# Optimization experiments

Measured on AMD Instinct MI355X. Metric: run time of the kernel, lower is better.

The kernel has to match this reference:

```python
import jax, jax.numpy as jnp
import numpy as np

K = 1024          # num_embeddings
D = 768           # embedding_dim
COMMIT = 0.25     # commitment_cost
PW = 0.1          # perplexity_weight


def setup_inputs() -> dict:
    key = jax.random.key(0)
    k1, k2 = jax.random.split(key)
    inputs = jax.random.normal(k1, (32, 2048, D), dtype=jnp.float32)
    weight = jax.random.normal(k2, (K, D), dtype=jnp.float32)  # codebook
    return {"inputs": inputs, "weight": weight}


def reference(inputs, weight):
    """Eval-mode forward of VectorQuantizerEMA (deterministic nearest-code lookup)."""
    in_shape = inputs.shape
    flat = inputs.reshape(-1, D)                       # [N, D]
    valid = jnp.linalg.norm(flat, axis=1) > 1e-6       # padding mask [N]
    maskf = valid.astype(flat.dtype)
    n_valid = maskf.sum()

    dist = (jnp.sum(flat * flat, axis=1, keepdims=True)
            + jnp.sum(weight * weight, axis=1)
            - 2.0 * flat @ weight.T)

    idx = jnp.argmin(dist, axis=1)                     # [N]
    min_d = jnp.min(dist, axis=1)                      # [N]
    idx = jnp.where(valid, idx, 0)
    min_d = jnp.where(valid, min_d, 0.0)

    q_flat = weight[idx] * maskf[:, None]              # zeros at padded rows
    quantized = q_flat.reshape(in_shape)
    quantized_st = inputs + jax.lax.stop_gradient(quantized - inputs)

    # commitment loss: MSE over valid rows only
    sq_err = jnp.sum((flat - jax.lax.stop_gradient(q_flat)) ** 2, axis=1)
    loss_commit = jnp.sum(maskf * sq_err) / (n_valid * D)

    # perplexity over valid assignments (one-hot mean == normalized counts)
    counts = jnp.zeros((K,), flat.dtype).at[idx].add(maskf)
    avg_probs = counts / n_valid
    perplexity = jnp.exp(-jnp.sum(avg_probs * jnp.log(avg_probs + 1e-10)))
    perplexity_loss = -jnp.log(perplexity + 1e-10)

    total_loss = COMMIT * loss_commit + PW * perplexity_loss

    indices = idx.reshape(in_shape[:-1])
    min_distances = min_d.reshape(in_shape[:-1])
    return quantized_st, total_loss, indices, min_distances, perplexity
```

## Files before the change

kernel.cpp:

```cpp
#include <hip/hip_runtime.h>
#include <hip/hip_bf16.h>
#include <math.h>

#define NROWS 65536
#define DDIM  768
#define KCODES 1024
#define NCB   8
#define BM    128
#define BK    128
#define KC    32
#define NCH   (DDIM / KC)
#define BK2   32
#define NCH2  (DDIM / BK2)
#define PANEL_USH (24 * 4096)
#define GAP_TAU  0.3f
#define FILT_TAU 0.6f
#define RGRID 2048
#define QGRID 2048

#define OUT_LOSS ((size_t)NROWS * DDIM)
#define OUT_IDX  (OUT_LOSS + 1)
#define OUT_MIND (OUT_IDX + NROWS)
#define OUT_PERP (OUT_MIND + NROWS)

#define WS_SUM    0
#define WS_NSUS   8
#define WS_NVAL   12
#define WS_COUNTS 256
#define WS_WSQ    (WS_COUNTS + 4*KCODES)
#define WS_ROWS   (WS_WSQ + 4*KCODES)
#define WS_ROWI   (WS_ROWS + 4*NROWS)
#define WS_SUSP   (WS_ROWI + 4*NROWS)
#define WS_PM1    (WS_SUSP + 4*NROWS)
#define WS_PM2    (WS_PM1 + (size_t)4*NROWS*NCB)
#define WS_PIDX   (WS_PM2 + (size_t)4*NROWS*NCB)
#define WS_END    (WS_PIDX + (size_t)4*NROWS*NCB)
#define WS_AF16   ((WS_END + 255) & ~(size_t)255)
#define WS_WF16   (WS_AF16 + (size_t)NROWS * DDIM * 2)
#define WS_END2   (WS_WF16 + (size_t)KCODES * DDIM * 2)

typedef __attribute__((ext_vector_type(8))) _Float16 half8;
typedef __attribute__((ext_vector_type(4))) float f32x4;

#define GLOAD16(gsrc, ldst) \
    __builtin_amdgcn_global_load_lds( \
        (const __attribute__((address_space(1))) unsigned int*)(gsrc), \
        (__attribute__((address_space(3))) unsigned int*)(ldst), 16, 0, 0)

template <typename T>
__device__ inline T waveRedAdd(T v) {
#pragma unroll
    for (int o = 32; o; o >>= 1) v += __shfl_xor(v, o);
    return v;
}

__device__ inline ushort f2h(float f) {
    union { _Float16 h; ushort u; } c;
    c.h = (_Float16)f;
    return c.u;
}

__global__ void k_init(float* counts, int* n_suspect, unsigned* n_valid, double* sum_sqerr) {
    const int t = threadIdx.x;
    if (t == 0) { *n_suspect = 0; *n_valid = 0u; *sum_sqerr = 0.0; }
    for (int k = t; k < KCODES; k += 256) counts[k] = 0.f;
}

#define ASLOTS (NROWS * (DDIM / 8))
#define TSLOTS ((NROWS + KCODES) * (DDIM / 8))
__global__ __launch_bounds__(256) void k_convert(
    const float* __restrict__ A, const float* __restrict__ W,
    ushort* __restrict__ Af16, ushort* __restrict__ Wf16)
{
    for (int gidx = blockIdx.x * 256 + threadIdx.x; gidx < TSLOTS; gidx += gridDim.x * 256) {
        const float* src; ushort* dst; int sid;
        if (gidx < ASLOTS) { src = A; dst = Af16; sid = gidx; }
        else { src = W; dst = Wf16; sid = gidx - ASLOTS; }
        const int row = sid / 96;
        const int sl = sid - row * 96;
        const int ch = sl >> 2, s = sl & 3;
        const float* p = src + (size_t)row * DDIM + ch * 32 + s * 8;
        const float4 a = *(const float4*)p;
        const float4 b = *(const float4*)(p + 4);
        uint4 v;
        v.x = ((unsigned)f2h(a.y) << 16) | f2h(a.x);
        v.y = ((unsigned)f2h(a.w) << 16) | f2h(a.z);
        v.z = ((unsigned)f2h(b.y) << 16) | f2h(b.x);
        v.w = ((unsigned)f2h(b.w) << 16) | f2h(b.z);
        const size_t dsti = (size_t)(row >> 7) * PANEL_USH + ch * 4096
                          + (row & 127) * 32 + ((s ^ ((row >> 1) & 3)) << 3);
        *(uint4*)(dst + dsti) = v;
    }
}

__global__ __launch_bounds__(256) void k_wsq(const float* __restrict__ W, float* __restrict__ wsq) {
    const int k = blockIdx.x;
    const int t = threadIdx.x;
    const float* w = W + (size_t)k * DDIM;
    const float a = w[t], b = w[t + 256], c = w[t + 512];
    float s = a * a + b * b + c * c;
    s = waveRedAdd(s);
    __shared__ float p[4];
    if ((t & 63) == 0) p[t >> 6] = s;
    __syncthreads();
    if (t == 0) wsq[k] = (p[0] + p[1]) + (p[2] + p[3]);
}

__global__ __launch_bounds__(256, 4) void k_partials_g(
    const ushort* __restrict__ Af16, const ushort* __restrict__ Wf16,
    const float* __restrict__ wsq,
    float* __restrict__ pm1, float* __restrict__ pm2, int* __restrict__ pidx)
{
    __shared__ __align__(16) ushort lds[2 * 2 * BM * BK2];

    const int bid = blockIdx.x;
    const int rb = ((bid & 7) << 6) | (bid >> 6);
    const int cb = (bid >> 3) & 7;

    const int tid = threadIdx.x;
    const int wid = tid >> 6, lane = tid & 63;
    const int wr = wid >> 1, wc = wid & 1;
    const int l15 = lane & 15, g = lane >> 4;

    const ushort* Ap = Af16 + (size_t)rb * PANEL_USH;
    const ushort* Wp = Wf16 + (size_t)cb * PANEL_USH;

    int aoff[4], boff[4];
#pragma unroll
    for (int rt = 0; rt < 4; ++rt) {
        const int r = wr * 64 + rt * 16 + l15;
        aoff[rt] = r * 32 + ((g ^ ((r >> 1) & 3)) << 3);
        const int c = wc * 64 + rt * 16 + l15;
        boff[rt] = c * 32 + ((g ^ ((c >> 1) & 3)) << 3);
    }

    f32x4 acc[4][4];
#pragma unroll
    for (int rt = 0; rt < 4; ++rt)
#pragma unroll
        for (int ct = 0; ct < 4; ++ct) acc[rt][ct] = (f32x4)0.f;

    const int lseg = lane << 3;
    auto STAGE = [&](int ch, int b) {
        ushort* As = lds + b * 8192;
        ushort* Ws = As + 4096;
        const ushort* Asrc = Ap + ch * 4096;
        const ushort* Wsrc = Wp + ch * 4096;
        GLOAD16(Asrc + (wid << 9) + lseg,       (char*)As + (wid << 10));
        GLOAD16(Asrc + ((wid + 4) << 9) + lseg, (char*)As + ((wid + 4) << 10));
        GLOAD16(Wsrc + (wid << 9) + lseg,       (char*)Ws + (wid << 10));
        GLOAD16(Wsrc + ((wid + 4) << 9) + lseg, (char*)Ws + ((wid + 4) << 10));
    };

    STAGE(0, 0);
    __syncthreads();

#pragma unroll 2
    for (int ch = 0; ch < NCH2; ++ch) {
        const int cur = ch & 1;
        if (ch + 1 < NCH2) STAGE(ch + 1, cur ^ 1);
        const ushort* As = lds + cur * 8192;
        const ushort* Ws = As + 4096;
        half8 bf[4];
#pragma unroll
        for (int ct = 0; ct < 4; ++ct) bf[ct] = *(const half8*)(Ws + boff[ct]);
#pragma unroll
        for (int rt = 0; rt < 4; ++rt) {
            const half8 af = *(const half8*)(As + aoff[rt]);
#pragma unroll
            for (int ct = 0; ct < 4; ++ct)
                acc[rt][ct] = __builtin_amdgcn_mfma_f32_16x16x32_f16(af, bf[ct], acc[rt][ct], 0, 0, 0);
        }
        __syncthreads();
    }

    float wq[4];
#pragma unroll
    for (int ct = 0; ct < 4; ++ct) wq[ct] = wsq[cb * BK + wc * 64 + ct * 16 + l15];
    const int cbase = cb * BK + wc * 64 + l15;

    float* tm1 = (float*)lds;
    float* tm2 = tm1 + 256;
    int*   ti1 = (int*)(tm2 + 256);

#pragma unroll
    for (int rt = 0; rt < 4; ++rt) {
        float m1q[4], m2q[4]; int i1q[4];
#pragma unroll
        for (int q = 0; q < 4; ++q) { m1q[q] = INFINITY; m2q[q] = INFINITY; i1q[q] = 0x7fffffff; }
#pragma unroll
        for (int ct = 0; ct < 4; ++ct) {
            const int col = cbase + ct * 16;
#pragma unroll
            for (int q = 0; q < 4; ++q) {
                const float s = fmaf(-2.f, acc[rt][ct][q], wq[ct]);
                if (s < m1q[q]) { m2q[q] = m1q[q]; m1q[q] = s; i1q[q] = col; }
                else if (s < m2q[q]) m2q[q] = s;
            }
        }
#pragma unroll
        for (int msk = 1; msk <= 8; msk <<= 1) {
#pragma unroll
            for (int q = 0; q < 4; ++q) {
                const float om1 = __shfl_xor(m1q[q], msk);
                const float om2 = __shfl_xor(m2q[q], msk);
                const int   oi1 = __shfl_xor(i1q[q], msk);
                if (om1 < m1q[q] || (om1 == m1q[q] && oi1 < i1q[q])) {
                    m2q[q] = fminf(m1q[q], om2); m1q[q] = om1; i1q[q] = oi1;
                } else m2q[q] = fminf(m2q[q], om1);
            }
        }
        if (l15 == 0) {
#pragma unroll
            for (int q = 0; q < 4; ++q) {
                const int rl = wr * 64 + rt * 16 + g * 4 + q;
                tm1[rl * 2 + wc] = m1q[q];
                tm2[rl * 2 + wc] = m2q[q];
                ti1[rl * 2 + wc] = i1q[q];
            }
        }
    }
    __syncthreads();
    if (tid < BM) {
        float m1 = tm1[tid * 2], m2 = tm2[tid * 2]; int i1 = ti1[tid * 2];
        const float bm1 = tm1[tid * 2 + 1], bm2 = tm2[tid * 2 + 1]; const int bi = ti1[tid * 2 + 1];
        if (bm1 < m1 || (bm1 == m1 && bi < i1)) { m2 = fminf(m1, bm2); m1 = bm1; i1 = bi; }
        else m2 = fminf(m2, bm1);
        const size_t row = (size_t)rb * BM + tid;
        pm1[row * NCB + cb] = m1;
        pm2[row * NCB + cb] = m2;
        pidx[row * NCB + cb] = i1;
    }
}

__global__ __launch_bounds__(256, 2) void k_partials(
    const float* __restrict__ A, const float* __restrict__ W,
    const float* __restrict__ wsq,
    float* __restrict__ pm1, float* __restrict__ pm2, int* __restrict__ pidx)
{
    __shared__ __align__(16) ushort lds[2 * BM * KC];
    ushort* As = lds;
    ushort* Ws = lds + BM * KC;

    const int bid = blockIdx.x;
    const int rb = ((bid & 7) << 6) | (bid >> 6);
    const int cb = (bid >> 3) & 7;

    const int tid = threadIdx.x;
    const int wid = tid >> 6, lane = tid & 63;
    const int wr = wid >> 1, wc = wid & 1;
    const int l15 = lane & 15, g = lane >> 4;

    const float* Ab = A + (size_t)rb * BM * DDIM;
    const float* Wb = W + (size_t)cb * BK * DDIM;

    const int srow = tid >> 3;
    const int sk4  = (tid & 7) << 2;
    const int sg   = (tid & 7) >> 1;
    const int sh   = (tid & 1) << 2;

    int aOff[4], bOff[4];
#pragma unroll
    for (int rt = 0; rt < 4; ++rt) {
        const int r = wr * 64 + rt * 16 + l15;
        aOff[rt] = r * KC + ((g ^ ((r >> 1) & 3)) << 3);
        const int c = wc * 64 + rt * 16 + l15;
        bOff[rt] = c * KC + ((g ^ ((c >> 1) & 3)) << 3);
    }

    f32x4 acc[4][4];
#pragma unroll
    for (int rt = 0; rt < 4; ++rt)
#pragma unroll
        for (int ct = 0; ct < 4; ++ct) acc[rt][ct] = (f32x4)0.f;

    float4 av[4], wv[4];
#pragma unroll
    for (int i = 0; i < 4; ++i) {
        av[i] = *(const float4*)(Ab + (size_t)(srow + 32 * i) * DDIM + sk4);
        wv[i] = *(const float4*)(Wb + (size_t)(srow + 32 * i) * DDIM + sk4);
    }

#pragma unroll 1
    for (int ch = 0; ch < NCH; ++ch) {
        __syncthreads();
#pragma unroll
        for (int i = 0; i < 4; ++i) {
            const int r = srow + 32 * i;
            const int wsl = r * KC + ((sg ^ ((r >> 1) & 3)) << 3) + sh;
            ushort4 ua; ua.x = f2h(av[i].x); ua.y = f2h(av[i].y); ua.z = f2h(av[i].z); ua.w = f2h(av[i].w);
            *(ushort4*)(As + wsl) = ua;
            ushort4 uw; uw.x = f2h(wv[i].x); uw.y = f2h(wv[i].y); uw.z = f2h(wv[i].z); uw.w = f2h(wv[i].w);
            *(ushort4*)(Ws + wsl) = uw;
        }
        __syncthreads();
        if (ch + 1 < NCH) {
            const int d0 = (ch + 1) * KC + sk4;
#pragma unroll
            for (int i = 0; i < 4; ++i) {
                av[i] = *(const float4*)(Ab + (size_t)(srow + 32 * i) * DDIM + d0);
                wv[i] = *(const float4*)(Wb + (size_t)(srow + 32 * i) * DDIM + d0);
            }
        }
        half8 af[4], bf[4];
#pragma unroll
        for (int rt = 0; rt < 4; ++rt) af[rt] = *(const half8*)(As + aOff[rt]);
#pragma unroll
        for (int ct = 0; ct < 4; ++ct) bf[ct] = *(const half8*)(Ws + bOff[ct]);
#pragma unroll
        for (int rt = 0; rt < 4; ++rt)
#pragma unroll
            for (int ct = 0; ct < 4; ++ct)
                acc[rt][ct] = __builtin_amdgcn_mfma_f32_16x16x32_f16(af[rt], bf[ct], acc[rt][ct], 0, 0, 0);
    }

    float wq[4];
#pragma unroll
    for (int ct = 0; ct < 4; ++ct) wq[ct] = wsq[cb * BK + wc * 64 + ct * 16 + l15];
    const int cbase = cb * BK + wc * 64 + l15;

    __syncthreads();
    float* tm1 = (float*)lds;
    float* tm2 = tm1 + 256;
    int*   ti1 = (int*)(tm2 + 256);

#pragma unroll
    for (int rt = 0; rt < 4; ++rt) {
        float m1q[4], m2q[4]; int i1q[4];
#pragma unroll
        for (int q = 0; q < 4; ++q) { m1q[q] = INFINITY; m2q[q] = INFINITY; i1q[q] = 0x7fffffff; }
#pragma unroll
        for (int ct = 0; ct < 4; ++ct) {
            const int col = cbase + ct * 16;
#pragma unroll
            for (int q = 0; q < 4; ++q) {
                const float s = fmaf(-2.f, acc[rt][ct][q], wq[ct]);
                if (s < m1q[q]) { m2q[q] = m1q[q]; m1q[q] = s; i1q[q] = col; }
                else if (s < m2q[q]) m2q[q] = s;
            }
        }
#pragma unroll
        for (int msk = 1; msk <= 8; msk <<= 1) {
#pragma unroll
            for (int q = 0; q < 4; ++q) {
                const float om1 = __shfl_xor(m1q[q], msk);
                const float om2 = __shfl_xor(m2q[q], msk);
                const int   oi1 = __shfl_xor(i1q[q], msk);
                if (om1 < m1q[q] || (om1 == m1q[q] && oi1 < i1q[q])) {
                    m2q[q] = fminf(m1q[q], om2); m1q[q] = om1; i1q[q] = oi1;
                } else m2q[q] = fminf(m2q[q], om1);
            }
        }
        if (l15 == 0) {
#pragma unroll
            for (int q = 0; q < 4; ++q) {
                const int rl = wr * 64 + rt * 16 + g * 4 + q;
                tm1[rl * 2 + wc] = m1q[q];
                tm2[rl * 2 + wc] = m2q[q];
                ti1[rl * 2 + wc] = i1q[q];
            }
        }
    }
    __syncthreads();
    if (tid < BM) {
        float m1 = tm1[tid * 2], m2 = tm2[tid * 2]; int i1 = ti1[tid * 2];
        const float bm1 = tm1[tid * 2 + 1], bm2 = tm2[tid * 2 + 1]; const int bi = ti1[tid * 2 + 1];
        if (bm1 < m1 || (bm1 == m1 && bi < i1)) { m2 = fminf(m1, bm2); m1 = bm1; i1 = bi; }
        else m2 = fminf(m2, bm1);
        const size_t row = (size_t)rb * BM + tid;
        pm1[row * NCB + cb] = m1;
        pm2[row * NCB + cb] = m2;
        pidx[row * NCB + cb] = i1;
    }
}

__global__ __launch_bounds__(256) void k_merge(
    const float* __restrict__ pm1, const float* __restrict__ pm2, const int* __restrict__ pidx,
    float* __restrict__ row_s, int* __restrict__ row_idx,
    int* __restrict__ suspects, int* __restrict__ n_suspect)
{
    const int row = blockIdx.x * 256 + threadIdx.x;
    float m1 = INFINITY, m2 = INFINITY; int i1 = 0x7fffffff;
#pragma unroll
    for (int cb = 0; cb < NCB; ++cb) {
        const float bm1 = pm1[(size_t)row * NCB + cb];
        const float bm2 = pm2[(size_t)row * NCB + cb];
        const int   bi  = pidx[(size_t)row * NCB + cb];
        if (bm1 < m1 || (bm1 == m1 && bi < i1)) { m2 = fminf(m1, bm2); m1 = bm1; i1 = bi; }
        else m2 = fminf(m2, bm1);
    }
    row_s[row] = m1;
    row_idx[row] = i1;
    if (m2 - m1 < GAP_TAU) {
        const int p = atomicAdd(n_suspect, 1);
        suspects[p] = row;
    }
}

__global__ __launch_bounds__(256) void k_repair(
    const float* __restrict__ A, const float* __restrict__ W,
    const float* __restrict__ pm1,
    const int* __restrict__ suspects, const int* __restrict__ n_suspect,
    float* __restrict__ row_s, int* __restrict__ row_idx)
{
    __shared__ __align__(16) float xrow[DDIM];
    __shared__ double wbest[4]; __shared__ int wbi[4];
    __shared__ double xps[4];
    __shared__ int qcb[NCB];
    __shared__ int nq;
    const int ns = *n_suspect;
    const int tid = threadIdx.x;
    const int wid = tid >> 6, lane = tid & 63;
    const int sub = tid & 3;
    const int cq  = tid >> 2;

    for (int s = blockIdx.x; s < ns; s += gridDim.x) {
        const int row = suspects[s];
        __syncthreads();
        xrow[tid]       = A[(size_t)row * DDIM + tid];
        xrow[tid + 256] = A[(size_t)row * DDIM + tid + 256];
        xrow[tid + 512] = A[(size_t)row * DDIM + tid + 512];
        if (tid == 0) {
            float gmin = INFINITY;
#pragma unroll
            for (int cb = 0; cb < NCB; ++cb) gmin = fminf(gmin, pm1[(size_t)row * NCB + cb]);
            int n = 0;
#pragma unroll
            for (int cb = 0; cb < NCB; ++cb)
                if (pm1[(size_t)row * NCB + cb] <= gmin + FILT_TAU) qcb[n++] = cb;
            nq = n;
        }
        __syncthreads();

        double xp = 0.0;
        {
            double t;
            t = (double)xrow[tid];       xp = fma(t, t, xp);
            t = (double)xrow[tid + 256]; xp = fma(t, t, xp);
            t = (double)xrow[tid + 512]; xp = fma(t, t, xp);
        }
        xp = waveRedAdd(xp);
        if (lane == 0) xps[wid] = xp;

        double best = 1e300; int bi = 0x7fffffff;
        const int ncand = nq * BK;
        for (int base = 0; base < ncand; base += 64) {
            const int ci = base + cq;
            const bool act = ci < ncand;
            double d = 0.0; int k = 0x7fffffff;
            if (act) {
                k = qcb[ci >> 7] * BK + (ci & (BK - 1));
                const float* wr = W + (size_t)k * DDIM + (sub << 2);
                const float* xr = xrow + (sub << 2);
                double d0 = 0.0, d1 = 0.0;
                for (int i = 0; i < DDIM; i += 16) {
                    const float4 wv = *(const float4*)(wr + i);
                    const float4 xv = *(const float4*)(xr + i);
                    double t;
                    t = (double)xv.x - (double)wv.x; d0 = fma(t, t, d0);
                    t = (double)xv.y - (double)wv.y; d1 = fma(t, t, d1);
                    t = (double)xv.z - (double)wv.z; d0 = fma(t, t, d0);
                    t = (double)xv.w - (double)wv.w; d1 = fma(t, t, d1);
                }
                d = d0 + d1;
            }
            d += __shfl_xor(d, 1);
            d += __shfl_xor(d, 2);
            if (act && sub == 0) {
                if (d < best || (d == best && k < bi)) { best = d; bi = k; }
            }
        }
#pragma unroll
        for (int o = 32; o; o >>= 1) {
            const double ob = __shfl_xor(best, o);
            const int oi = __shfl_xor(bi, o);
            if (ob < best || (ob == best && oi < bi)) { best = ob; bi = oi; }
        }
        if (lane == 0) { wbest[wid] = best; wbi[wid] = bi; }
        __syncthreads();
        if (tid == 0) {
            double b = wbest[0]; int i1 = wbi[0];
#pragma unroll
            for (int w = 1; w < 4; ++w)
                if (wbest[w] < b || (wbest[w] == b && wbi[w] < i1)) { b = wbest[w]; i1 = wbi[w]; }
            row_idx[row] = i1;
            row_s[row] = (float)(b - (xps[0] + xps[1] + xps[2] + xps[3]));
        }
    }
}

__global__ __launch_bounds__(256) void k_quantize(
    const float* __restrict__ A, const float* __restrict__ W,
    const float* __restrict__ row_s, const int* __restrict__ row_idx,
    float* __restrict__ out, float* __restrict__ counts,
    unsigned int* __restrict__ n_valid, double* __restrict__ sum_sqerr)
{
    const int wid = threadIdx.x >> 6, lane = threadIdx.x & 63;
    __shared__ double s_sum[4];
    __shared__ unsigned s_val[4];
    double wsum = 0.0; unsigned wval = 0;

#pragma unroll 1
    for (int it = 0; it < NROWS / (QGRID * 4); ++it) {
        const int row = (it * QGRID + blockIdx.x) * 4 + wid;
        const float* x = A + (size_t)row * DDIM;
        float4 xv[3];
#pragma unroll
        for (int j = 0; j < 3; ++j) xv[j] = *(const float4*)(x + (lane + 64 * j) * 4);
        float xsq = 0.f;
#pragma unroll
        for (int j = 0; j < 3; ++j)
            xsq += xv[j].x * xv[j].x + xv[j].y * xv[j].y + xv[j].z * xv[j].z + xv[j].w * xv[j].w;
        xsq = waveRedAdd(xsq);
        const bool valid = xsq > 1e-12f;
        const float maskf = valid ? 1.f : 0.f;
        const int idx = row_idx[row];
        const int idxm = valid ? idx : 0;
        const float* w = W + (size_t)idx * DDIM;
        float* oq = out + (size_t)row * DDIM;
        float e2 = 0.f;
#pragma unroll
        for (int j = 0; j < 3; ++j) {
            const float4 wvv = *(const float4*)(w + (lane + 64 * j) * 4);
            const float xs[4] = {xv[j].x, xv[j].y, xv[j].z, xv[j].w};
            const float ws[4] = {wvv.x, wvv.y, wvv.z, wvv.w};
            float os[4];
#pragma unroll
            for (int c = 0; c < 4; ++c) {
                const float q = ws[c] * maskf;
                os[c] = xs[c] + (q - xs[c]);
                const float d = xs[c] - q;
                e2 += d * d;
            }
            float4 ov; ov.x = os[0]; ov.y = os[1]; ov.z = os[2]; ov.w = os[3];
            *(float4*)(oq + (lane + 64 * j) * 4) = ov;
        }
        e2 = waveRedAdd(e2);
        if (lane == 0) {
            wsum += (double)(maskf * e2);
            if (valid) {
                ++wval;
                atomicAdd(&counts[idxm], 1.0f);
            }
            out[OUT_IDX + row]  = (float)idxm;
            out[OUT_MIND + row] = valid ? (xsq + row_s[row]) : 0.f;
        }
    }

    if (lane == 0) { s_sum[wid] = wsum; s_val[wid] = wval; }
    __syncthreads();
    if (threadIdx.x == 0) {
        atomicAdd(sum_sqerr, s_sum[0] + s_sum[1] + s_sum[2] + s_sum[3]);
        atomicAdd(n_valid, s_val[0] + s_val[1] + s_val[2] + s_val[3]);
    }
}

__global__ __launch_bounds__(256) void k_final(
    const float* __restrict__ counts, const unsigned int* __restrict__ n_valid,
    const double* __restrict__ sum_sqerr, float* __restrict__ out)
{
    const int t = threadIdx.x;
    const float nv = (float)(*n_valid);
    double ent = 0.0;
    for (int k = t; k < KCODES; k += 256) {
        const float p = counts[k] / nv;
        ent += (double)(p * logf(p + 1e-10f));
    }
    ent = waveRedAdd(ent);
    __shared__ double ps[4];
    if ((t & 63) == 0) ps[t >> 6] = ent;
    __syncthreads();
    if (t == 0) {
        const double e = ps[0] + ps[1] + ps[2] + ps[3];
        const double perp = exp(-e);
        const double ploss = -log(perp + 1e-10);
        const double commit = *sum_sqerr / ((double)(*n_valid) * (double)DDIM);
        out[OUT_LOSS] = (float)(0.25 * commit + 0.1 * ploss);
        out[OUT_PERP] = (float)perp;
    }
}

extern "C" void kernel_launch(void* const* d_in, const int* in_sizes, int n_in,
                              void* d_out, int out_size, void* d_ws, size_t ws_size,
                              hipStream_t stream) {
    const float* A = (const float*)d_in[0];
    const float* W = (const float*)d_in[1];
    float* out = (float*)d_out;
    char* ws = (char*)d_ws;
    if (ws_size < (size_t)WS_END) return;

    double*   sum_sqerr = (double*)(ws + WS_SUM);
    int*      n_suspect = (int*)(ws + WS_NSUS);
    unsigned* n_valid   = (unsigned*)(ws + WS_NVAL);
    float*    counts    = (float*)(ws + WS_COUNTS);
    float*    wsq       = (float*)(ws + WS_WSQ);
    float*    row_s     = (float*)(ws + WS_ROWS);
    int*      row_idx   = (int*)(ws + WS_ROWI);
    int*      suspects  = (int*)(ws + WS_SUSP);
    float*    pm1       = (float*)(ws + WS_PM1);
    float*    pm2       = (float*)(ws + WS_PM2);
    int*      pidx      = (int*)(ws + WS_PIDX);
    ushort*   Af16      = (ushort*)(ws + WS_AF16);
    ushort*   Wf16      = (ushort*)(ws + WS_WF16);

    const bool big = ws_size >= (size_t)WS_END2;

    hipLaunchKernelGGL(k_init, dim3(1), dim3(256), 0, stream, counts, n_suspect, n_valid, sum_sqerr);
    if (big)
        hipLaunchKernelGGL(k_convert, dim3(2048), dim3(256), 0, stream, A, W, Af16, Wf16);
    hipLaunchKernelGGL(k_wsq, dim3(KCODES), dim3(256), 0, stream, W, wsq);
    if (big)
        hipLaunchKernelGGL(k_partials_g, dim3((NROWS / BM) * NCB), dim3(256), 0, stream, Af16, Wf16, wsq, pm1, pm2, pidx);
    else
        hipLaunchKernelGGL(k_partials, dim3((NROWS / BM) * NCB), dim3(256), 0, stream, A, W, wsq, pm1, pm2, pidx);
    hipLaunchKernelGGL(k_merge, dim3(NROWS / 256), dim3(256), 0, stream, pm1, pm2, pidx, row_s, row_idx, suspects, n_suspect);
    hipLaunchKernelGGL(k_repair, dim3(RGRID), dim3(256), 0, stream, A, W, pm1, suspects, n_suspect, row_s, row_idx);
    hipLaunchKernelGGL(k_quantize, dim3(QGRID), dim3(256), 0, stream, A, W, row_s, row_idx, out, counts, n_valid, sum_sqerr);
    hipLaunchKernelGGL(k_final, dim3(1), dim3(256), 0, stream, counts, n_valid, sum_sqerr, out);
}
```

Before: 364.9 us.

## Load GEMM fragments directly from global into registers, dropping LDS staging

The distance GEMM kernel no longer stages A and W chunks through LDS with global_load_lds and barriers. Each wave now reads its MFMA fragments straight from the pre-swizzled global panels into registers, prefetching the next chunk into a second register set. The launch-bounds occupancy hint drops from 4 to 3 to make room for the extra registers. This removes the per-chunk syncs and the LDS traffic, but the data each wave shares through LDS is now read separately from global or cache by every wave, and more registers are needed.

```diff
diff --git a/kernel.cpp b/kernel.cpp
--- a/kernel.cpp
+++ b/kernel.cpp
@@ -41,11 +41,6 @@
 
 typedef __attribute__((ext_vector_type(8))) _Float16 half8;
 typedef __attribute__((ext_vector_type(4))) float f32x4;
-
-#define GLOAD16(gsrc, ldst) \
-    __builtin_amdgcn_global_load_lds( \
-        (const __attribute__((address_space(1))) unsigned int*)(gsrc), \
-        (__attribute__((address_space(3))) unsigned int*)(ldst), 16, 0, 0)
 
 template <typename T>
 __device__ inline T waveRedAdd(T v) {
@@ -106,12 +101,12 @@
     if (t == 0) wsq[k] = (p[0] + p[1]) + (p[2] + p[3]);
 }
 
-__global__ __launch_bounds__(256, 4) void k_partials_g(
+__global__ __launch_bounds__(256, 3) void k_partials_g(
     const ushort* __restrict__ Af16, const ushort* __restrict__ Wf16,
     const float* __restrict__ wsq,
     float* __restrict__ pm1, float* __restrict__ pm2, int* __restrict__ pidx)
 {
-    __shared__ __align__(16) ushort lds[2 * 2 * BM * BK2];
+    __shared__ float smem[768];
 
     const int bid = blockIdx.x;
     const int rb = ((bid & 7) << 6) | (bid >> 6);
@@ -140,38 +135,32 @@
 #pragma unroll
         for (int ct = 0; ct < 4; ++ct) acc[rt][ct] = (f32x4)0.f;
 
-    const int lseg = lane << 3;
-    auto STAGE = [&](int ch, int b) {
-        ushort* As = lds + b * 8192;
-        ushort* Ws = As + 4096;
-        const ushort* Asrc = Ap + ch * 4096;
-        const ushort* Wsrc = Wp + ch * 4096;
-        GLOAD16(Asrc + (wid << 9) + lseg,       (char*)As + (wid << 10));
-        GLOAD16(Asrc + ((wid + 4) << 9) + lseg, (char*)As + ((wid + 4) << 10));
-        GLOAD16(Wsrc + (wid << 9) + lseg,       (char*)Ws + (wid << 10));
-        GLOAD16(Wsrc + ((wid + 4) << 9) + lseg, (char*)Ws + ((wid + 4) << 10));
-    };
-
-    STAGE(0, 0);
-    __syncthreads();
-
-#pragma unroll 2
+    half8 afp[4], bfp[4];
+#pragma unroll
+    for (int rt = 0; rt < 4; ++rt) afp[rt] = *(const half8*)(Ap + aoff[rt]);
+#pragma unroll
+    for (int ct = 0; ct < 4; ++ct) bfp[ct] = *(const half8*)(Wp + boff[ct]);
+
+#pragma unroll 1
     for (int ch = 0; ch < NCH2; ++ch) {
-        const int cur = ch & 1;
-        if (ch + 1 < NCH2) STAGE(ch + 1, cur ^ 1);
-        const ushort* As = lds + cur * 8192;
-        const ushort* Ws = As + 4096;
-        half8 bf[4];
-#pragma unroll
-        for (int ct = 0; ct < 4; ++ct) bf[ct] = *(const half8*)(Ws + boff[ct]);
-#pragma unroll
-        for (int rt = 0; rt < 4; ++rt) {
-            const half8 af = *(const half8*)(As + aoff[rt]);
+        half8 afc[4], bfc[4];
+#pragma unroll
+        for (int rt = 0; rt < 4; ++rt) afc[rt] = afp[rt];
+#pragma unroll
+        for (int ct = 0; ct < 4; ++ct) bfc[ct] = bfp[ct];
+        if (ch + 1 < NCH2) {
+            const ushort* An = Ap + (ch + 1) * 4096;
+            const ushort* Wn = Wp + (ch + 1) * 4096;
+#pragma unroll
+            for (int rt = 0; rt < 4; ++rt) afp[rt] = *(const half8*)(An + aoff[rt]);
+#pragma unroll
+            for (int ct = 0; ct < 4; ++ct) bfp[ct] = *(const half8*)(Wn + boff[ct]);
+        }
+#pragma unroll
+        for (int rt = 0; rt < 4; ++rt)
 #pragma unroll
             for (int ct = 0; ct < 4; ++ct)
-                acc[rt][ct] = __builtin_amdgcn_mfma_f32_16x16x32_f16(af, bf[ct], acc[rt][ct], 0, 0, 0);
-        }
-        __syncthreads();
+                acc[rt][ct] = __builtin_amdgcn_mfma_f32_16x16x32_f16(afc[rt], bfc[ct], acc[rt][ct], 0, 0, 0);
     }
 
     float wq[4];
@@ -179,7 +168,7 @@
     for (int ct = 0; ct < 4; ++ct) wq[ct] = wsq[cb * BK + wc * 64 + ct * 16 + l15];
     const int cbase = cb * BK + wc * 64 + l15;
 
-    float* tm1 = (float*)lds;
+    float* tm1 = smem;
     float* tm2 = tm1 + 256;
     int*   ti1 = (int*)(tm2 + 256);
 
```

Result: slower. 374.7 us (+2.7%).
